# Kernel tuning notes

Measured on AMD Instinct MI355X. Metric: run time of the kernel, lower is better.

The kernel has to match this reference:

```python
import jax, jax.numpy as jnp
import numpy as np

EPS = 1e-8
NUM_HEADS = 8
SCALE = 25.0
SIM_THRESH = 0.75
BLOCK = 10  # per-frame proposal group size used by the zeroing mask


def _l2norm(x):
    return x / (jnp.linalg.norm(x, axis=-1, keepdims=True) + EPS)


def setup_inputs() -> dict:
    key = jax.random.key(0)
    ks = jax.random.split(key, 7)
    B, N, C = 1, 2000, 256
    H = NUM_HEADS
    x_cls = jax.random.normal(ks[0], (B, N, C), dtype=jnp.float32)
    x_reg = jax.random.normal(ks[1], (B, N, C), dtype=jnp.float32)
    cls_score = jax.random.uniform(ks[2], (N,), dtype=jnp.float32)
    fg_score = jax.random.uniform(ks[3], (N,), dtype=jnp.float32)
    coord_attn = jax.random.uniform(ks[4], (B, H, N, N), dtype=jnp.float32)
    W_qkv_cls = jax.random.normal(ks[5], (3 * C, C), dtype=jnp.float32) * 0.02
    W_qkv_reg = jax.random.normal(ks[6], (3 * C, C), dtype=jnp.float32) * 0.02
    return {"x_cls": x_cls, "x_reg": x_reg, "cls_score": cls_score,
            "fg_score": fg_score, "coord_attn": coord_attn,
            "W_qkv_cls": W_qkv_cls, "W_qkv_reg": W_qkv_reg}


def reference(x_cls, x_reg, cls_score, fg_score, coord_attn, W_qkv_cls, W_qkv_reg):
    B, N, C = x_cls.shape
    H = NUM_HEADS
    D = C // H

    def qkv(x, W):
        t = (x @ W.T).reshape(B, N, 3, H, D).transpose(2, 0, 3, 1, 4)  # [3,B,H,N,D]
        return t[0], t[1], t[2]

    q_cls, k_cls, v_cls = qkv(x_cls, W_qkv_cls)
    q_reg, k_reg, v_reg = qkv(x_reg, W_qkv_reg)

    q_cls, k_cls = _l2norm(q_cls), _l2norm(k_cls)
    q_reg, k_reg = _l2norm(q_reg), _l2norm(k_reg)
    v_cls_normed = _l2norm(v_cls)

    cs = cls_score.reshape(1, 1, 1, N)  # broadcast over [B,H,N,N]
    fs = fg_score.reshape(1, 1, 1, N)

    attn_cls_raw = jnp.einsum('bhnd,bhmd->bhnm', v_cls_normed, v_cls_normed)

    attn_cls = jax.nn.softmax(jnp.einsum('bhnd,bhmd->bhnm', q_cls, k_cls) * SCALE * cs, axis=-1)
    attn_reg = jax.nn.softmax(jnp.einsum('bhnd,bhmd->bhnm', q_reg, k_reg) * SCALE * fs, axis=-1)

    attn = (attn_reg + attn_cls) * 0.5 * coord_attn
    attn = jax.lax.stop_gradient(attn)  # original detaches before masking

    # block-diagonal zeroing: row j zeros cols [j//10*10, j//10*10+9), keep diagonal
    rows = jnp.arange(N)[:, None]
    cols = jnp.arange(N)[None, :]
    block_start = (rows // BLOCK) * BLOCK
    zero_mask = (cols >= block_start) & (cols < block_start + (BLOCK - 1)) & (cols != rows)
    attn = jnp.where(zero_mask, 0.0, attn)

    x = jnp.einsum('bhnm,bhmd->bhnd', attn, v_cls).transpose(0, 2, 1, 3).reshape(B, N, C)
    x_ori = v_cls.transpose(0, 2, 1, 3).reshape(B, N, C)
    x_cat = jnp.concatenate([x, x_ori], axis=-1)  # [B,N,2C]

    # ave=True branch
    sim_raw = jnp.sum(attn_cls_raw, axis=1)[0] / H          # [N,N]
    sim_mask = (sim_raw > SIM_THRESH).astype(x_cls.dtype)
    sim_attn = jnp.sum(attn, axis=1)[0] / H                 # [N,N]
    sim_round2 = jax.nn.softmax(sim_attn, axis=-1)
    sim_round2 = sim_mask * sim_round2 / (jnp.sum(sim_mask * sim_round2, axis=-1, keepdims=True) + EPS)
    return x_cat, sim_round2
```

## Files before the change

kernel.cpp:

```cpp
#include <hip/hip_runtime.h>
#include <math.h>

typedef _Float16 half8 __attribute__((ext_vector_type(8)));
typedef _Float16 half4 __attribute__((ext_vector_type(4)));
typedef _Float16 half2v __attribute__((ext_vector_type(2)));
typedef float f32x4 __attribute__((ext_vector_type(4)));

constexpr int N = 2000;
constexpr int NP = 2048;
constexpr int H = 8;
constexpr int D = 32;
constexpr float SCL = 25.0f;
constexpr float L2E = 1.4426950408889634f;
constexpr float FM2 = 25.0f * L2E;

#define MFMA16(a,b,c)  __builtin_amdgcn_mfma_f32_16x16x32_f16((a),(b),(c),0,0,0)
#define MFMA16K(a,b,c) __builtin_amdgcn_mfma_f32_16x16x16f16((a),(b),(c),0,0,0)

__device__ __forceinline__ float fexp2(float x) { return __builtin_amdgcn_exp2f(x); }


__global__ __launch_bounds__(256) void wconv_kernel(
    const float* __restrict__ Wc, const float* __restrict__ Wr,
    _Float16* __restrict__ Wch, _Float16* __restrict__ Wrh)
{
    const int i = blockIdx.x * 256 + threadIdx.x;
    Wch[i] = (_Float16)Wc[i];
    Wrh[i] = (_Float16)Wr[i];
}

__global__ __launch_bounds__(256) void qkv_kernel(
    const float* __restrict__ xc, const float* __restrict__ xr,
    const _Float16* __restrict__ Wch, const _Float16* __restrict__ Wrh,
    const float* __restrict__ clsScore, const float* __restrict__ fgScore,
    _Float16* __restrict__ Qch, _Float16* __restrict__ Kch,
    _Float16* __restrict__ Qrh, _Float16* __restrict__ Krh,
    _Float16* __restrict__ Vnh, _Float16* __restrict__ Vth,
    float* __restrict__ out)
{
    constexpr int XS = 264;
    __shared__ _Float16 xs[16 * XS];
    const int t = threadIdx.x;
    const int n0 = blockIdx.x * 16;
    const int by = blockIdx.y;
    const int which = (by < 3) ? by : (by - 3);
    const bool isCls = by < 3;
    const float* x = isCls ? xc : xr;
    const _Float16* Wh = isCls ? Wch : Wrh;

    #pragma unroll
    for (int it = 0; it < 4; ++it) {
        const int f = t + it * 256;
        const int row = f >> 6, c4 = f & 63;
        const float4 v = *(const float4*)(x + (size_t)(n0 + row) * 256 + c4 * 4);
        half4 hv; hv[0]=(_Float16)v.x; hv[1]=(_Float16)v.y; hv[2]=(_Float16)v.z; hv[3]=(_Float16)v.w;
        *(half4*)&xs[row * XS + c4 * 4] = hv;
    }
    __syncthreads();

    const int w = t >> 6, l = t & 63;
    const int lr = l & 15, lg = l >> 4;
    const int obase = which * 256 + w * 64;
    f32x4 acc[4] = {{0,0,0,0},{0,0,0,0},{0,0,0,0},{0,0,0,0}};
    for (int k0 = 0; k0 < 256; k0 += 32) {
        const half8 aX = *(const half8*)&xs[lr * XS + k0 + lg * 8];
        #pragma unroll
        for (int s = 0; s < 4; ++s) {
            const half8 bW = *(const half8*)(Wh + (size_t)(obase + s * 16 + lr) * 256 + k0 + lg * 8);
            acc[s] = MFMA16(aX, bW, acc[s]);
        }
    }
    f32x4 kscale = {1.f,1.f,1.f,1.f};
    if (which == 1) {
        const float* sp = isCls ? clsScore : fgScore;
        kscale = (SCL * L2E) * *(const f32x4*)(sp + n0 + lg*4);
    }
    #pragma unroll
    for (int p = 0; p < 2; ++p) {
        const int h = 2 * w + p;
        float ss[4];
        #pragma unroll
        for (int j = 0; j < 4; ++j) {
            float v = acc[2*p][j]*acc[2*p][j] + acc[2*p+1][j]*acc[2*p+1][j];
            #pragma unroll
            for (int off = 1; off < 16; off <<= 1) v += __shfl_xor(v, off);
            ss[j] = sqrtf(v) + 1e-8f;
        }
        if (which < 2) {
            _Float16* Qd = isCls ? (which == 0 ? Qch : Kch) : (which == 0 ? Qrh : Krh);
            #pragma unroll
            for (int sh = 0; sh < 2; ++sh)
                #pragma unroll
                for (int j = 0; j < 4; ++j)
                    Qd[((size_t)h*NP + n0 + lg*4 + j)*D + sh*16 + lr]
                        = (_Float16)(acc[2*p+sh][j] / ss[j] * kscale[j]);
        } else {
            #pragma unroll
            for (int sh = 0; sh < 2; ++sh) {
                const int d = sh * 16 + lr;
                half4 tv;
                #pragma unroll
                for (int j = 0; j < 4; ++j) {
                    const float raw = acc[2*p+sh][j];
                    Vnh[((size_t)h*NP + n0 + lg*4 + j)*D + d] = (_Float16)(raw / ss[j]);
                    out[(size_t)(n0 + lg*4 + j)*512 + 256 + h*D + d] = raw;
                    tv[j] = (_Float16)raw;
                }
                *(half4*)(Vth + ((size_t)h*D + d)*NP + n0 + lg*4) = tv;
            }
        }
    }
}

__global__ __launch_bounds__(512) void stats_kernel(
    const _Float16* __restrict__ Qch, const _Float16* __restrict__ Kch,
    const _Float16* __restrict__ Qrh, const _Float16* __restrict__ Krh,
    float* __restrict__ BIAS)
{
    __shared__ float Ssh[2][4][16];
    const int t = threadIdx.x;
    const int w = t >> 6, l = t & 63;
    const int nsub = w >> 2, mq = w & 3;
    const int n0 = blockIdx.x * 32 + nsub * 16;
    const int h = blockIdx.y, z = blockIdx.z;
    const _Float16* Q = z ? Qrh : Qch;
    const _Float16* K = z ? Krh : Kch;
    const int lr = l & 15, lg = l >> 4;
    const half8 aQ = *(const half8*)(Q + ((size_t)h*NP + n0 + lr)*D + lg*8);
    float S[4] = {0.f, 0.f, 0.f, 0.f};
    const int mqB0 = (mq == 0) ? 0 : 31*mq;
    const int mqB1 = (mq == 3) ? 125 : 31*(mq+1);
    half8 bK = *(const half8*)(K + ((size_t)h*NP + mqB0*16 + lr)*D + lg*8);
    for (int ms = mqB0; ms < mqB1; ++ms) {
        const half8 cur = bK;
        if (ms + 1 < mqB1)
            bK = *(const half8*)(K + ((size_t)h*NP + (ms+1)*16 + lr)*D + lg*8);
        f32x4 z4 = {0.f, 0.f, 0.f, 0.f};
        const f32x4 c = MFMA16(aQ, cur, z4);
        #pragma unroll
        for (int j = 0; j < 4; ++j) S[j] += fexp2(c[j] - FM2);
    }
    #pragma unroll
    for (int j = 0; j < 4; ++j) {
        #pragma unroll
        for (int off = 1; off < 16; off <<= 1) S[j] += __shfl_xor(S[j], off);
    }
    if (lr == 0) {
        #pragma unroll
        for (int j = 0; j < 4; ++j) Ssh[nsub][mq][lg*4 + j] = S[j];
    }
    __syncthreads();
    if (t < 32) {
        const int ns = t >> 4, rl = t & 15;
        const int n = blockIdx.x * 32 + ns*16 + rl;
        BIAS[((size_t)z*H + h)*NP + n]
            = -__log2f(Ssh[ns][0][rl] + Ssh[ns][1][rl] + Ssh[ns][2][rl] + Ssh[ns][3][rl]) - FM2 - 1.0f;
    }
}

__global__ __launch_bounds__(256) void vvmask_kernel(
    const _Float16* __restrict__ Vnh, unsigned char* __restrict__ Mask)
{
    const int t = threadIdx.x;
    const int w = t >> 6, l = t & 63;
    const int n0 = blockIdx.y * 16;
    const int m00 = blockIdx.x * 256 + w * 64;
    const int lr = l & 15, lg = l >> 4;
    half8 aV[8];
    #pragma unroll
    for (int h = 0; h < 8; ++h)
        aV[h] = *(const half8*)(Vnh + ((size_t)(h*NP + n0 + lr))*D + lg*8);
    for (int s = 0; s < 4; ++s) {
        const int mb = m00 + s*16;
        f32x4 acc = {0.f, 0.f, 0.f, 0.f};
        #pragma unroll
        for (int h = 0; h < 8; ++h) {
            const half8 bV = *(const half8*)(Vnh + ((size_t)(h*NP + mb + lr))*D + lg*8);
            acc = MFMA16(aV[h], bV, acc);
        }
        const int m = mb + lr;
        if (m < N) {
            #pragma unroll
            for (int j = 0; j < 4; ++j) {
                const int n = n0 + lg*4 + j;
                Mask[(size_t)n*N + m] = (acc[j]*0.125f > 0.75f) ? (unsigned char)1 : (unsigned char)0;
            }
        }
    }
}

template<int SMAX>
__global__ __launch_bounds__(256, 5) void attn_kernel(
    const _Float16* __restrict__ Kch, const _Float16* __restrict__ Krh,
    const _Float16* __restrict__ Qch, const _Float16* __restrict__ Qrh,
    const _Float16* __restrict__ Vth, const float* __restrict__ coord,
    const float* __restrict__ BIAS,
    _Float16* __restrict__ SIMH, _Float16* __restrict__ XPH, int mcBase)
{
    __shared__ _Float16 simred[4][16][136];

    const int t = threadIdx.x;
    const int w = t >> 6, l = t & 63;
    const int lr = l & 15, lg = l >> 4;
    const int mc = mcBase + blockIdx.x;
    const int m0 = mc * 128;
    const int n0 = blockIdx.y * 16;
    const int n = n0 + lr;
    const int bs = (n / 10) * 10;
    const int h0 = 2 * w;

    unsigned kill = 0u;
    #pragma unroll
    for (int s = 0; s < SMAX; ++s)
        #pragma unroll
        for (int j = 0; j < 4; ++j) {
            const int m = m0 + s*16 + lg*4 + j;
            if (m >= bs && m < bs + 9 && m != n) kill |= (1u << (s*4 + j));
        }

    half8 aQc[2], aQr[2]; float bC[2], bR[2];
    #pragma unroll
    for (int p = 0; p < 2; ++p) {
        const int h = h0 + p;
        aQc[p] = *(const half8*)(Qch + ((size_t)h*NP + n)*D + lg*8);
        aQr[p] = *(const half8*)(Qrh + ((size_t)h*NP + n)*D + lg*8);
        bC[p] = BIAS[(size_t)h*NP + n];
        bR[p] = BIAS[(size_t)(H + h)*NP + n];
    }

    half2v sacc[SMAX][2];
    #pragma unroll
    for (int s = 0; s < SMAX; ++s)
        #pragma unroll
        for (int k = 0; k < 2; ++k) { sacc[s][k][0] = (_Float16)0.f; sacc[s][k][1] = (_Float16)0.f; }

    half8 kc[2], kr[2]; half4 v0[2], v1[2]; f32x4 co[3];
    auto LOADCO = [&](int it) {
        const int p = it / SMAX, s = it % SMAX, c = it % 3;
        const int h = h0 + p;
        co[c] = *(const f32x4*)(coord + ((size_t)h*N + n)*N + m0 + s*16 + lg*4);
    };
    auto LOADKV = [&](int it) {
        const int p = it / SMAX, s = it % SMAX, b = it & 1;
        const int h = h0 + p;
        const size_t kb = ((size_t)h*NP + m0 + s*16 + lr)*D + lg*8;
        kc[b] = *(const half8*)(Kch + kb);
        kr[b] = *(const half8*)(Krh + kb);
        v0[b] = *(const half4*)(Vth + ((size_t)(h*D + lr))*NP + m0 + s*16 + lg*4);
        v1[b] = *(const half4*)(Vth + ((size_t)(h*D + 16 + lr))*NP + m0 + s*16 + lg*4);
    };

    f32x4 pv0 = {0,0,0,0}, pv1 = {0,0,0,0};
    LOADCO(0);
    if (2*SMAX > 1) LOADCO(1);
    LOADKV(0);
    #pragma unroll
    for (int it = 0; it < 2*SMAX; ++it) {
        const int p = it / SMAX, s = it % SMAX, b = it & 1, c = it % 3;
        if (it + 2 < 2*SMAX) LOADCO(it + 2);
        if (it + 1 < 2*SMAX) LOADKV(it + 1);
        f32x4 z4 = {0.f,0.f,0.f,0.f};
        const f32x4 cc = MFMA16(kc[b], aQc[p], z4);
        const f32x4 cr = MFMA16(kr[b], aQr[p], z4);
        half4 af;
        #pragma unroll
        for (int j = 0; j < 4; ++j) {
            float a = (fexp2(cc[j] + bC[p]) + fexp2(cr[j] + bR[p])) * co[c][j];
            if ((kill >> (s*4 + j)) & 1u) a = 0.f;
            af[j] = (_Float16)a;
        }
        sacc[s][0] += (half2v){af[0], af[1]};
        sacc[s][1] += (half2v){af[2], af[3]};
        pv0 = MFMA16K(af, v0[b], pv0);
        pv1 = MFMA16K(af, v1[b], pv1);
        if (s == SMAX - 1) {
            const int h = h0 + p;
            _Float16* xp = XPH + (((size_t)(mc*H + h)*N + n0 + lg*4))*D + lr;
            #pragma unroll
            for (int j = 0; j < 4; ++j) {
                xp[j*D]      = (_Float16)pv0[j];
                xp[j*D + 16] = (_Float16)pv1[j];
            }
            pv0 = (f32x4){0,0,0,0}; pv1 = (f32x4){0,0,0,0};
        }
    }

    #pragma unroll
    for (int s = 0; s < SMAX; ++s) {
        half4 sv; sv[0]=sacc[s][0][0]; sv[1]=sacc[s][0][1]; sv[2]=sacc[s][1][0]; sv[3]=sacc[s][1][1];
        *(half4*)&simred[w][lr][s*16 + lg*4] = sv;
    }
    __syncthreads();
    constexpr int C8 = SMAX * 2;
    for (int e = t; e < 16 * C8; e += 256) {
        const int r = e / C8, c8 = e % C8;
        const half8 s0 = *(const half8*)&simred[0][r][c8*8];
        const half8 s1 = *(const half8*)&simred[1][r][c8*8];
        const half8 s2 = *(const half8*)&simred[2][r][c8*8];
        const half8 s3 = *(const half8*)&simred[3][r][c8*8];
        const half8 sum = (s0 + s1) + (s2 + s3);
        *(half8*)(SIMH + (size_t)(n0 + r)*N + m0 + c8*8) = sum;
    }
}

__global__ __launch_bounds__(256) void reduce_kernel(
    const _Float16* __restrict__ XPH, float* __restrict__ out)
{
    const int n = blockIdx.x, t = threadIdx.x;
    const int h = t >> 5, d = t & 31;
    float acc = 0.f;
    #pragma unroll
    for (int mcI = 0; mcI < 16; ++mcI)
        acc += (float)XPH[(((size_t)mcI*H + h)*N + n)*D + d];
    out[(size_t)n*512 + t] = acc;
}

__global__ __launch_bounds__(256) void simfinal_kernel(
    const _Float16* __restrict__ SIMH, const unsigned char* __restrict__ Mask,
    float* __restrict__ out)
{
    __shared__ float redA[4], redB[4];
    const int n = blockIdx.x, t = threadIdx.x;
    const _Float16* row = SIMH + (size_t)n * N;
    const unsigned char* mrow = Mask + (size_t)n * N;
    const bool act = t < 250;
    float f[8];
    unsigned int mk0 = 0, mk1 = 0;
    float mx = -1e30f;
    if (act) {
        const half8 v8 = *(const half8*)(row + t*8);
        const uint2 mm = *(const uint2*)(mrow + t*8);
        mk0 = mm.x; mk1 = mm.y;
        #pragma unroll
        for (int k = 0; k < 8; ++k) { f[k] = (float)v8[k]; mx = fmaxf(mx, f[k]); }
    }
    #pragma unroll
    for (int off = 1; off < 64; off <<= 1) mx = fmaxf(mx, __shfl_xor(mx, off));
    const int wv = t >> 6;
    if ((t & 63) == 0) redA[wv] = mx;
    __syncthreads();
    const float M = fmaxf(fmaxf(redA[0], redA[1]), fmaxf(redA[2], redA[3]));
    float e[8];
    float sA = 0.f, sM = 0.f;
    if (act) {
        #pragma unroll
        for (int k = 0; k < 8; ++k) {
            e[k] = fexp2((f[k] - M) * (L2E * 0.125f));
            sA += e[k];
            const unsigned int mkb = ((k < 4 ? mk0 : mk1) >> (8*(k & 3))) & 0xffu;
            if (mkb) sM += e[k]; else e[k] = 0.f;
        }
    }
    #pragma unroll
    for (int off = 1; off < 64; off <<= 1) { sA += __shfl_xor(sA, off); sM += __shfl_xor(sM, off); }
    __syncthreads();
    if ((t & 63) == 0) { redA[wv] = sA; redB[wv] = sM; }
    __syncthreads();
    const float SA = redA[0] + redA[1] + redA[2] + redA[3];
    const float SMK = redB[0] + redB[1] + redB[2] + redB[3];
    const float inv = 1.f / (SMK + 1e-8f * SA);
    if (act) {
        float* orow = out + 1024000 + (size_t)n*N + t*8;
        *(float4*)(orow)     = make_float4(e[0]*inv, e[1]*inv, e[2]*inv, e[3]*inv);
        *(float4*)(orow + 4) = make_float4(e[4]*inv, e[5]*inv, e[6]*inv, e[7]*inv);
    }
}

extern "C" void kernel_launch(void* const* d_in, const int* in_sizes, int n_in,
                              void* d_out, int out_size, void* d_ws, size_t ws_size,
                              hipStream_t stream) {
    const float* x_cls     = (const float*)d_in[0];
    const float* x_reg     = (const float*)d_in[1];
    const float* cls_score = (const float*)d_in[2];
    const float* fg_score  = (const float*)d_in[3];
    const float* coord     = (const float*)d_in[4];
    const float* Wc        = (const float*)d_in[5];
    const float* Wr        = (const float*)d_in[6];

    char* base = (char*)d_ws;
    float* BIAS     = (float*)base;
    _Float16* SIMH  = (_Float16*)(base + 131072);
    _Float16* XPH   = (_Float16*)(base + 8131072);
    _Float16* Qch   = (_Float16*)(base + 24515072);
    _Float16* Kch   = Qch + 524288;
    _Float16* Qrh   = Qch + 2*524288;
    _Float16* Krh   = Qch + 3*524288;
    _Float16* Vnh   = Qch + 4*524288;
    _Float16* Vth   = Qch + 5*524288;
    _Float16* Wch   = (_Float16*)(base + 30806528);
    _Float16* Wrh   = (_Float16*)(base + 31199744);
    unsigned char* Mask = (unsigned char*)(base + 31592960);
    float* out = (float*)d_out;

    wconv_kernel<<<768, 256, 0, stream>>>(Wc, Wr, Wch, Wrh);
    qkv_kernel<<<dim3(125, 5), 256, 0, stream>>>(x_cls, x_reg, Wch, Wrh, cls_score, fg_score,
                                                 Qch, Kch, Qrh, Krh, Vnh, Vth, out);
    stats_kernel<<<dim3(63, 8, 2), 512, 0, stream>>>(Qch, Kch, Qrh, Krh, BIAS);
    vvmask_kernel<<<dim3(8, 125), 256, 0, stream>>>(Vnh, Mask);
    attn_kernel<8><<<dim3(15, 125), 256, 0, stream>>>(Kch, Krh, Qch, Qrh, Vth, coord,
                                                      BIAS, SIMH, XPH, 0);
    attn_kernel<5><<<dim3(1, 125), 256, 0, stream>>>(Kch, Krh, Qch, Qrh, Vth, coord,
                                                     BIAS, SIMH, XPH, 15);
    reduce_kernel<<<2000, 256, 0, stream>>>(XPH, out);
    simfinal_kernel<<<2000, 256, 0, stream>>>(SIMH, Mask, out);
}
```

Baseline: 136.2 us.

## Stage coord_attn tiles through LDS with coalesced row loads and prefetch

Coordinate-attention values were previously loaded straight into registers in MFMA fragment layout, which reads 16-byte pieces spread across 16 rows. Each wave now issues row-contiguous loads of a 16x64 coord chunk, one chunk ahead, writes it into a padded per-wave LDS buffer, and reads the fragment from LDS. The aim is better global coalescing and more latency hiding for the dominant coord stream. In exchange it adds about 17KB of LDS per block and LDS traffic, and it drops the occupancy hint from the launch bounds, so occupancy may fall.

```diff
diff --git a/kernel.cpp b/kernel.cpp
--- a/kernel.cpp
+++ b/kernel.cpp
@@ -190,13 +190,15 @@
 }
 
 template<int SMAX>
-__global__ __launch_bounds__(256, 5) void attn_kernel(
+__global__ __launch_bounds__(256) void attn_kernel(
     const _Float16* __restrict__ Kch, const _Float16* __restrict__ Krh,
     const _Float16* __restrict__ Qch, const _Float16* __restrict__ Qrh,
     const _Float16* __restrict__ Vth, const float* __restrict__ coord,
     const float* __restrict__ BIAS,
     _Float16* __restrict__ SIMH, _Float16* __restrict__ XPH, int mcBase)
 {
+    constexpr int CHW = 68;
+    __shared__ float costage[4][16 * CHW];
     __shared__ _Float16 simred[4][16][136];
 
     const int t = threadIdx.x;
@@ -209,6 +211,8 @@
     const int bs = (n / 10) * 10;
     const int h0 = 2 * w;
 
+    constexpr int NCH = (SMAX + 3) / 4;
+
     unsigned kill = 0u;
     #pragma unroll
     for (int s = 0; s < SMAX; ++s)
@@ -234,12 +238,41 @@
         #pragma unroll
         for (int k = 0; k < 2; ++k) { sacc[s][k][0] = (_Float16)0.f; sacc[s][k][1] = (_Float16)0.f; }
 
-    half8 kc[2], kr[2]; half4 v0[2], v1[2]; f32x4 co[3];
-    auto LOADCO = [&](int it) {
-        const int p = it / SMAX, s = it % SMAX, c = it % 3;
+    float* myco = &costage[w][0];
+    f32x4 creg[4];
+
+    auto ISSUE = [&](int ci) {
+        const int p = ci / NCH, g = ci % NCH;
         const int h = h0 + p;
-        co[c] = *(const f32x4*)(coord + ((size_t)h*N + n)*N + m0 + s*16 + lg*4);
+        const int nc = (SMAX - 4*g >= 4) ? 4 : (SMAX - 4*g);
+        const size_t rb = ((size_t)h*N + n0)*N + m0 + g*64;
+        if (nc == 4) {
+            #pragma unroll
+            for (int i = 0; i < 4; ++i) {
+                const int row = 4*i + (l >> 4), col = (l & 15)*4;
+                creg[i] = *(const f32x4*)(coord + rb + (size_t)row*N + col);
+            }
+        } else {
+            const int row = l >> 2, col = (l & 3)*4;
+            creg[0] = *(const f32x4*)(coord + rb + (size_t)row*N + col);
+        }
     };
+    auto WRITE = [&](int ci) {
+        const int g = ci % NCH;
+        const int nc = (SMAX - 4*g >= 4) ? 4 : (SMAX - 4*g);
+        if (nc == 4) {
+            #pragma unroll
+            for (int i = 0; i < 4; ++i) {
+                const int row = 4*i + (l >> 4), col = (l & 15)*4;
+                *(f32x4*)(myco + row*CHW + col) = creg[i];
+            }
+        } else {
+            const int row = l >> 2, col = (l & 3)*4;
+            *(f32x4*)(myco + row*CHW + col) = creg[0];
+        }
+    };
+
+    half8 kc[2], kr[2]; half4 v0[2], v1[2];
     auto LOADKV = [&](int it) {
         const int p = it / SMAX, s = it % SMAX, b = it & 1;
         const int h = h0 + p;
@@ -251,38 +284,48 @@
     };
 
     f32x4 pv0 = {0,0,0,0}, pv1 = {0,0,0,0};
-    LOADCO(0);
-    if (2*SMAX > 1) LOADCO(1);
+    ISSUE(0);
+    WRITE(0);
     LOADKV(0);
     #pragma unroll
-    for (int it = 0; it < 2*SMAX; ++it) {
-        const int p = it / SMAX, s = it % SMAX, b = it & 1, c = it % 3;
-        if (it + 2 < 2*SMAX) LOADCO(it + 2);
-        if (it + 1 < 2*SMAX) LOADKV(it + 1);
-        f32x4 z4 = {0.f,0.f,0.f,0.f};
-        const f32x4 cc = MFMA16(kc[b], aQc[p], z4);
-        const f32x4 cr = MFMA16(kr[b], aQr[p], z4);
-        half4 af;
-        #pragma unroll
-        for (int j = 0; j < 4; ++j) {
-            float a = (fexp2(cc[j] + bC[p]) + fexp2(cr[j] + bR[p])) * co[c][j];
-            if ((kill >> (s*4 + j)) & 1u) a = 0.f;
-            af[j] = (_Float16)a;
-        }
-        sacc[s][0] += (half2v){af[0], af[1]};
-        sacc[s][1] += (half2v){af[2], af[3]};
-        pv0 = MFMA16K(af, v0[b], pv0);
-        pv1 = MFMA16K(af, v1[b], pv1);
-        if (s == SMAX - 1) {
-            const int h = h0 + p;
-            _Float16* xp = XPH + (((size_t)(mc*H + h)*N + n0 + lg*4))*D + lr;
+    for (int ci = 0; ci < 2*NCH; ++ci) {
+        const int p = ci / NCH, g = ci % NCH;
+        if (ci + 1 < 2*NCH) ISSUE(ci + 1);
+        __builtin_amdgcn_sched_barrier(0);
+        const int sBeg = 4*g;
+        const int sEnd = (SMAX - 4*g >= 4) ? (4*g + 4) : SMAX;
+        #pragma unroll
+        for (int s = sBeg; s < sEnd; ++s) {
+            const int it = p*SMAX + s;
+            const int b = it & 1;
+            if (it + 1 < 2*SMAX) LOADKV(it + 1);
+            const f32x4 co = *(const f32x4*)(myco + lr*CHW + (s - sBeg)*16 + lg*4);
+            f32x4 z4 = {0.f,0.f,0.f,0.f};
+            const f32x4 cc = MFMA16(kc[b], aQc[p], z4);
+            const f32x4 cr = MFMA16(kr[b], aQr[p], z4);
+            half4 af;
             #pragma unroll
             for (int j = 0; j < 4; ++j) {
-                xp[j*D]      = (_Float16)pv0[j];
-                xp[j*D + 16] = (_Float16)pv1[j];
-            }
-            pv0 = (f32x4){0,0,0,0}; pv1 = (f32x4){0,0,0,0};
-        }
+                float a = (fexp2(cc[j] + bC[p]) + fexp2(cr[j] + bR[p])) * co[j];
+                if ((kill >> (s*4 + j)) & 1u) a = 0.f;
+                af[j] = (_Float16)a;
+            }
+            sacc[s][0] += (half2v){af[0], af[1]};
+            sacc[s][1] += (half2v){af[2], af[3]};
+            pv0 = MFMA16K(af, v0[b], pv0);
+            pv1 = MFMA16K(af, v1[b], pv1);
+            if (s == SMAX - 1) {
+                const int h = h0 + p;
+                _Float16* xp = XPH + (((size_t)(mc*H + h)*N + n0 + lg*4))*D + lr;
+                #pragma unroll
+                for (int j = 0; j < 4; ++j) {
+                    xp[j*D]      = (_Float16)pv0[j];
+                    xp[j*D + 16] = (_Float16)pv1[j];
+                }
+                pv0 = (f32x4){0,0,0,0}; pv1 = (f32x4){0,0,0,0};
+            }
+        }
+        if (ci + 1 < 2*NCH) WRITE(ci + 1);
     }
 
     #pragma unroll
```

After: 133.8 us. No clear change (-1.7%).

## Restructure attention kernel: split columns across waves, async LDS staging of coord

Applied to the files above, without the earlier changes.

The attention kernel now gives each wave a slice of the 128 columns and loops over all 8 heads, where before each wave handled two heads over every column. The coord tile for the next head is fetched straight into swizzled LDS with global_load_lds, double-buffered, while the current head is computed. Per-head PV partials are reduced across waves through LDS, and the similarity sums stay in fp32 registers, which removes the old cross-wave LDS reduction. The two launches for the tail block become one launch, using clamped addresses and kill masks for columns past N, at the cost of a block barrier per head.

```diff
diff --git a/kernel.cpp b/kernel.cpp
--- a/kernel.cpp
+++ b/kernel.cpp
@@ -189,117 +189,138 @@
     }
 }
 
-template<int SMAX>
-__global__ __launch_bounds__(256, 5) void attn_kernel(
+__global__ __launch_bounds__(256) void attn_kernel(
     const _Float16* __restrict__ Kch, const _Float16* __restrict__ Krh,
     const _Float16* __restrict__ Qch, const _Float16* __restrict__ Qrh,
     const _Float16* __restrict__ Vth, const float* __restrict__ coord,
     const float* __restrict__ BIAS,
-    _Float16* __restrict__ SIMH, _Float16* __restrict__ XPH, int mcBase)
-{
-    __shared__ _Float16 simred[4][16][136];
+    _Float16* __restrict__ SIMH, _Float16* __restrict__ XPH)
+{
+    __shared__ __align__(16) float costage[2][2048];
+    __shared__ _Float16 pvred[2][4][2][16][18];
 
     const int t = threadIdx.x;
     const int w = t >> 6, l = t & 63;
     const int lr = l & 15, lg = l >> 4;
-    const int mc = mcBase + blockIdx.x;
+    const int mc = blockIdx.x;
     const int m0 = mc * 128;
     const int n0 = blockIdx.y * 16;
-    const int n = n0 + lr;
+    const int n  = n0 + lr;
     const int bs = (n / 10) * 10;
-    const int h0 = 2 * w;
+    const int s0 = w * 2;
 
     unsigned kill = 0u;
     #pragma unroll
-    for (int s = 0; s < SMAX; ++s)
+    for (int sl = 0; sl < 2; ++sl)
         #pragma unroll
         for (int j = 0; j < 4; ++j) {
-            const int m = m0 + s*16 + lg*4 + j;
-            if (m >= bs && m < bs + 9 && m != n) kill |= (1u << (s*4 + j));
-        }
+            const int m = m0 + (s0 + sl)*16 + lg*4 + j;
+            if ((m >= bs && m < bs + 9 && m != n) || m >= N) kill |= (1u << (sl*4 + j));
+        }
+
+    const int drow = w*4 + (l >> 4);
+    const int dck  = l & 15;
+    auto DMACO = [&](int hp) {
+        float* dst = &costage[hp & 1][0];
+        #pragma unroll
+        for (int i = 0; i < 2; ++i) {
+            const int colb = i*64 + ((((dck*16) ^ ((drow & 7) << 4))) >> 2);
+            unsigned gi = (unsigned)((hp*N + (n0 + drow))*N + m0 + colb);
+            gi = gi < 31999996u ? gi : 31999996u;
+            __builtin_amdgcn_global_load_lds(
+                (const __attribute__((address_space(1))) void*)(coord + gi),
+                (__attribute__((address_space(3))) void*)(dst + i*1024 + w*256),
+                16, 0, 0);
+        }
+    };
 
     half8 aQc[2], aQr[2]; float bC[2], bR[2];
-    #pragma unroll
-    for (int p = 0; p < 2; ++p) {
-        const int h = h0 + p;
-        aQc[p] = *(const half8*)(Qch + ((size_t)h*NP + n)*D + lg*8);
-        aQr[p] = *(const half8*)(Qrh + ((size_t)h*NP + n)*D + lg*8);
-        bC[p] = BIAS[(size_t)h*NP + n];
-        bR[p] = BIAS[(size_t)(H + h)*NP + n];
-    }
-
-    half2v sacc[SMAX][2];
-    #pragma unroll
-    for (int s = 0; s < SMAX; ++s)
-        #pragma unroll
-        for (int k = 0; k < 2; ++k) { sacc[s][k][0] = (_Float16)0.f; sacc[s][k][1] = (_Float16)0.f; }
-
-    half8 kc[2], kr[2]; half4 v0[2], v1[2]; f32x4 co[3];
-    auto LOADCO = [&](int it) {
-        const int p = it / SMAX, s = it % SMAX, c = it % 3;
-        const int h = h0 + p;
-        co[c] = *(const f32x4*)(coord + ((size_t)h*N + n)*N + m0 + s*16 + lg*4);
+    auto LOADQ = [&](int hp) {
+        const int hb = hp & 1;
+        aQc[hb] = *(const half8*)(Qch + ((size_t)hp*NP + n)*D + lg*8);
+        aQr[hb] = *(const half8*)(Qrh + ((size_t)hp*NP + n)*D + lg*8);
+        bC[hb]  = BIAS[(size_t)hp*NP + n];
+        bR[hb]  = BIAS[(size_t)(H + hp)*NP + n];
     };
-    auto LOADKV = [&](int it) {
-        const int p = it / SMAX, s = it % SMAX, b = it & 1;
-        const int h = h0 + p;
-        const size_t kb = ((size_t)h*NP + m0 + s*16 + lr)*D + lg*8;
+
+    half8 kc[2], kr[2]; half4 v0[2], v1[2];
+    auto LOADKV = [&](int hp, int sl, int b) {
+        const int m = m0 + (s0 + sl)*16;
+        const size_t kb = ((size_t)hp*NP + m + lr)*D + lg*8;
         kc[b] = *(const half8*)(Kch + kb);
         kr[b] = *(const half8*)(Krh + kb);
-        v0[b] = *(const half4*)(Vth + ((size_t)(h*D + lr))*NP + m0 + s*16 + lg*4);
-        v1[b] = *(const half4*)(Vth + ((size_t)(h*D + 16 + lr))*NP + m0 + s*16 + lg*4);
+        v0[b] = *(const half4*)(Vth + ((size_t)(hp*D + lr))*NP + m + lg*4);
+        v1[b] = *(const half4*)(Vth + ((size_t)(hp*D + 16 + lr))*NP + m + lg*4);
     };
 
-    f32x4 pv0 = {0,0,0,0}, pv1 = {0,0,0,0};
-    LOADCO(0);
-    if (2*SMAX > 1) LOADCO(1);
-    LOADKV(0);
-    #pragma unroll
-    for (int it = 0; it < 2*SMAX; ++it) {
-        const int p = it / SMAX, s = it % SMAX, b = it & 1, c = it % 3;
-        if (it + 2 < 2*SMAX) LOADCO(it + 2);
-        if (it + 1 < 2*SMAX) LOADKV(it + 1);
-        f32x4 z4 = {0.f,0.f,0.f,0.f};
-        const f32x4 cc = MFMA16(kc[b], aQc[p], z4);
-        const f32x4 cr = MFMA16(kr[b], aQr[p], z4);
-        half4 af;
-        #pragma unroll
-        for (int j = 0; j < 4; ++j) {
-            float a = (fexp2(cc[j] + bC[p]) + fexp2(cr[j] + bR[p])) * co[c][j];
-            if ((kill >> (s*4 + j)) & 1u) a = 0.f;
-            af[j] = (_Float16)a;
-        }
-        sacc[s][0] += (half2v){af[0], af[1]};
-        sacc[s][1] += (half2v){af[2], af[3]};
-        pv0 = MFMA16K(af, v0[b], pv0);
-        pv1 = MFMA16K(af, v1[b], pv1);
-        if (s == SMAX - 1) {
-            const int h = h0 + p;
-            _Float16* xp = XPH + (((size_t)(mc*H + h)*N + n0 + lg*4))*D + lr;
+    float sacc[2][4] = {{0,0,0,0},{0,0,0,0}};
+
+    DMACO(0); LOADQ(0);
+    __builtin_amdgcn_sched_barrier(0);
+    LOADKV(0, 0, 0);
+    asm volatile("s_waitcnt vmcnt(4)" ::: "memory");
+    __builtin_amdgcn_s_barrier();
+    __builtin_amdgcn_sched_barrier(0);
+
+    #pragma unroll
+    for (int h = 0; h < H; ++h) {
+        const int hb = h & 1;
+        if (h + 1 < H) { DMACO(h + 1); LOADQ(h + 1); }
+        __builtin_amdgcn_sched_barrier(0);
+        f32x4 pv0 = {0,0,0,0}, pv1 = {0,0,0,0};
+        #pragma unroll
+        for (int sl = 0; sl < 2; ++sl) {
+            const int b = (h*2 + sl) & 1;
+            if (sl == 0)            LOADKV(h, 1, b ^ 1);
+            else if (h + 1 < H)     LOADKV(h + 1, 0, b ^ 1);
+            const int s = s0 + sl;
+            const int cbyte = (((s & 3)*64 + lg*16) ^ ((lr & 7) << 4));
+            const f32x4 co = *(const f32x4*)(&costage[hb][(s >> 2)*1024 + lr*64] + (cbyte >> 2));
+            f32x4 z4 = {0,0,0,0};
+            const f32x4 cc = MFMA16(kc[b], aQc[hb], z4);
+            const f32x4 cr = MFMA16(kr[b], aQr[hb], z4);
+            half4 af;
             #pragma unroll
             for (int j = 0; j < 4; ++j) {
-                xp[j*D]      = (_Float16)pv0[j];
-                xp[j*D + 16] = (_Float16)pv1[j];
+                float a = (fexp2(cc[j] + bC[hb]) + fexp2(cr[j] + bR[hb])) * co[j];
+                if ((kill >> (sl*4 + j)) & 1u) a = 0.f;
+                sacc[sl][j] += a;
+                af[j] = (_Float16)a;
             }
-            pv0 = (f32x4){0,0,0,0}; pv1 = (f32x4){0,0,0,0};
-        }
-    }
-
-    #pragma unroll
-    for (int s = 0; s < SMAX; ++s) {
-        half4 sv; sv[0]=sacc[s][0][0]; sv[1]=sacc[s][0][1]; sv[2]=sacc[s][1][0]; sv[3]=sacc[s][1][1];
-        *(half4*)&simred[w][lr][s*16 + lg*4] = sv;
-    }
-    __syncthreads();
-    constexpr int C8 = SMAX * 2;
-    for (int e = t; e < 16 * C8; e += 256) {
-        const int r = e / C8, c8 = e % C8;
-        const half8 s0 = *(const half8*)&simred[0][r][c8*8];
-        const half8 s1 = *(const half8*)&simred[1][r][c8*8];
-        const half8 s2 = *(const half8*)&simred[2][r][c8*8];
-        const half8 s3 = *(const half8*)&simred[3][r][c8*8];
-        const half8 sum = (s0 + s1) + (s2 + s3);
-        *(half8*)(SIMH + (size_t)(n0 + r)*N + m0 + c8*8) = sum;
+            pv0 = MFMA16K(af, v0[b], pv0);
+            pv1 = MFMA16K(af, v1[b], pv1);
+        }
+        {
+            half4 h0v, h1v;
+            #pragma unroll
+            for (int j = 0; j < 4; ++j) { h0v[j] = (_Float16)pv0[j]; h1v[j] = (_Float16)pv1[j]; }
+            *(half4*)&pvred[hb][w][0][lr][lg*4] = h0v;
+            *(half4*)&pvred[hb][w][1][lr][lg*4] = h1v;
+        }
+        asm volatile("s_waitcnt vmcnt(4) lgkmcnt(0)" ::: "memory");
+        __builtin_amdgcn_s_barrier();
+        __builtin_amdgcn_sched_barrier(0);
+        {
+            const int e0 = 2*t;
+            const int d = e0 & 15, db = (e0 >> 4) & 1, q = e0 >> 5;
+            const float u0 = (float)pvred[hb][0][db][d][q]   + (float)pvred[hb][1][db][d][q]
+                           + (float)pvred[hb][2][db][d][q]   + (float)pvred[hb][3][db][d][q];
+            const float u1 = (float)pvred[hb][0][db][d+1][q] + (float)pvred[hb][1][db][d+1][q]
+                           + (float)pvred[hb][2][db][d+1][q] + (float)pvred[hb][3][db][d+1][q];
+            half2v o; o[0] = (_Float16)u0; o[1] = (_Float16)u1;
+            *(half2v*)(XPH + ((size_t)(mc*H + h)*N + n0)*D + e0) = o;
+        }
+    }
+
+    #pragma unroll
+    for (int sl = 0; sl < 2; ++sl) {
+        const int mbase = m0 + (s0 + sl)*16;
+        if (mbase < N) {
+            half4 sv;
+            #pragma unroll
+            for (int j = 0; j < 4; ++j) sv[j] = (_Float16)sacc[sl][j];
+            *(half4*)(SIMH + (size_t)n*N + mbase + lg*4) = sv;
+        }
     }
 }
 
@@ -397,10 +418,8 @@
                                                  Qch, Kch, Qrh, Krh, Vnh, Vth, out);
     stats_kernel<<<dim3(63, 8, 2), 512, 0, stream>>>(Qch, Kch, Qrh, Krh, BIAS);
     vvmask_kernel<<<dim3(8, 125), 256, 0, stream>>>(Vnh, Mask);
-    attn_kernel<8><<<dim3(15, 125), 256, 0, stream>>>(Kch, Krh, Qch, Qrh, Vth, coord,
-                                                      BIAS, SIMH, XPH, 0);
-    attn_kernel<5><<<dim3(1, 125), 256, 0, stream>>>(Kch, Krh, Qch, Qrh, Vth, coord,
-                                                     BIAS, SIMH, XPH, 15);
+    attn_kernel<<<dim3(16, 125), 256, 0, stream>>>(Kch, Krh, Qch, Qrh, Vth, coord,
+                                                   BIAS, SIMH, XPH);
     reduce_kernel<<<2000, 256, 0, stream>>>(XPH, out);
     simfinal_kernel<<<2000, 256, 0, stream>>>(SIMH, Mask, out);
 }
```

New measurement: 134.6 us. About the same (-1.2%).
